# Kernel tuning notes

Measured on AMD Instinct MI355X. Metric: run time of the kernel, lower is better.

The kernel has to match this reference:

```python
import jax, jax.numpy as jnp
import numpy as np

B, S, H = 16, 8192, 256


def setup_inputs() -> dict:
    key = jax.random.key(0)
    k1, k2, k3, k4, k5, k6 = jax.random.split(key, 6)
    # He/Glorot-ish scaling for the linear layer is irrelevant for correctness; use small randn.
    return {
        "query": jax.random.normal(k1, (B, 1, H), dtype=jnp.float32),
        "key": jax.random.normal(k2, (B, S, H), dtype=jnp.float32),
        "value": jax.random.normal(k3, (B, S, H), dtype=jnp.float32),
        "W_attn": jax.random.normal(k4, (H, 2 * H), dtype=jnp.float32) * 0.05,  # nn.Linear(2H, H).weight
        "b_attn": jax.random.normal(k5, (H,), dtype=jnp.float32) * 0.05,
        "v": jax.random.uniform(k6, (H,), dtype=jnp.float32),  # torch.rand init
    }


def reference(query, key, value, W_attn, b_attn, v):
    # Faithful to: tanh(Linear(cat([query.repeat(S), key], -1))) @ v -> softmax -> weighted sum.
    # Split the Linear weight so we never materialize the repeated/concatenated [B,S,2H] tensor:
    # cat([q,k]) @ W.T == q @ Wq.T + k @ Wk.T, with Wq = W[:, :H], Wk = W[:, H:].
    Wq = W_attn[:, :H]  # [H, H]
    Wk = W_attn[:, H:]  # [H, H]
    hidden = jnp.tanh(
        jnp.einsum("bqh,oh->bqo", query, Wq)        # [B,1,H], broadcasts over S
        + jnp.einsum("bsh,oh->bso", key, Wk)        # [B,S,H]
        + b_attn
    )  # [B,S,H]
    scores = jnp.einsum("bsh,h->bs", hidden, v)      # [B,S]
    attn_weights = jax.nn.softmax(scores, axis=-1)   # softmax over sequence
    context = jnp.einsum("bs,bsh->bh", attn_weights, value)[:, None, :]  # [B,1,H]
    return context, attn_weights
```

## Files before the change

### kernel.cpp

```cpp
#include <hip/hip_runtime.h>

#define B_SZ 16
#define S_SZ 8192
#define H_SZ 256

typedef _Float16 half8 __attribute__((ext_vector_type(8)));
typedef float f32x4 __attribute__((ext_vector_type(4)));

__device__ __forceinline__ float tanh_fast(float x) {
  float e = __expf(2.0f * x);
  return 1.0f - 2.0f / (e + 1.0f);
}

__global__ __launch_bounds__(256) void prep_kernel(
    const float* __restrict__ query, const float* __restrict__ W_attn,
    const float* __restrict__ b_attn, float* __restrict__ qb) {
  const int b = blockIdx.x;
  const int jo = blockIdx.y;
  const int wid = threadIdx.x >> 6;
  const int lane = threadIdx.x & 63;
  const float4 q4 = *(const float4*)(query + b * H_SZ + lane * 4);
#pragma unroll 4
  for (int i = 0; i < 16; i++) {
    const int o = jo * 64 + wid * 16 + i;
    const float4 w = *(const float4*)(W_attn + (size_t)o * 512 + lane * 4);
    float p = q4.x * w.x + q4.y * w.y + q4.z * w.z + q4.w * w.w;
#pragma unroll
    for (int off = 32; off >= 1; off >>= 1) p += __shfl_xor(p, off, 64);
    if (lane == 0) qb[b * H_SZ + o] = p + b_attn[o];
  }
}

__global__ __launch_bounds__(512, 4) void scores_kernel(
    const float* __restrict__ key, const float* __restrict__ W_attn,
    const float* __restrict__ qb, const float* __restrict__ vvec,
    float* __restrict__ scores) {
  __shared__ _Float16 lds[64 * 264];

  const int tid = threadIdx.x;
  const int wid = tid >> 6;
  const int lane = tid & 63;
  const int n = lane & 15;
  const int quad = lane >> 4;
  const int rowBase = blockIdx.x * 128;
  const int b = rowBase >> 13;
  const int r = rowBase + wid * 16 + n;

  const float* krow = key + (size_t)r * H_SZ + quad * 8;
  half8 afrag[8];
#pragma unroll
  for (int ks = 0; ks < 8; ks++) {
    const float4* p = (const float4*)(krow + ks * 32);
    float4 f0 = p[0];
    float4 f1 = p[1];
    half8 a;
    a[0] = (_Float16)f0.x; a[1] = (_Float16)f0.y;
    a[2] = (_Float16)f0.z; a[3] = (_Float16)f0.w;
    a[4] = (_Float16)f1.x; a[5] = (_Float16)f1.y;
    a[6] = (_Float16)f1.z; a[7] = (_Float16)f1.w;
    afrag[ks] = a;
  }

  float score[4] = {0.f, 0.f, 0.f, 0.f};

  for (int c = 0; c < 4; c++) {
    __syncthreads();
    for (int idx = tid; idx < 2048; idx += 512) {
      int row = idx >> 5, seg = idx & 31;
      const float4* src =
          (const float4*)(W_attn + (size_t)(c * 64 + row) * 512 + 256 + seg * 8);
      float4 f0 = src[0];
      float4 f1 = src[1];
      half8 h;
      h[0] = (_Float16)f0.x; h[1] = (_Float16)f0.y;
      h[2] = (_Float16)f0.z; h[3] = (_Float16)f0.w;
      h[4] = (_Float16)f1.x; h[5] = (_Float16)f1.y;
      h[6] = (_Float16)f1.z; h[7] = (_Float16)f1.w;
      *(half8*)&lds[row * 264 + seg * 8] = h;
    }
    __syncthreads();

    f32x4 acc[4];
#pragma unroll
    for (int t = 0; t < 4; t++) {
      f32x4 z = {0.f, 0.f, 0.f, 0.f};
      acc[t] = z;
    }

#pragma unroll
    for (int ks = 0; ks < 8; ks++) {
#pragma unroll
      for (int t = 0; t < 4; t++) {
        half8 bfrag =
            *(const half8*)&lds[(t * 16 + n) * 264 + ks * 32 + quad * 8];
        acc[t] = __builtin_amdgcn_mfma_f32_16x16x32_f16(afrag[ks], bfrag,
                                                        acc[t], 0, 0, 0);
      }
    }

#pragma unroll
    for (int t = 0; t < 4; t++) {
      const int tt = c * 4 + t;
      const float qbv = qb[b * H_SZ + tt * 16 + n];
      const float vv = vvec[tt * 16 + n];
#pragma unroll
      for (int rg = 0; rg < 4; rg++) {
        float hv = tanh_fast(qbv + acc[t][rg]);
        score[rg] = fmaf(vv, hv, score[rg]);
      }
    }
  }

#pragma unroll
  for (int rg = 0; rg < 4; rg++) {
#pragma unroll
    for (int m = 8; m >= 1; m >>= 1)
      score[rg] += __shfl_xor(score[rg], m, 64);
  }
  if (n == 0) {
#pragma unroll
    for (int rg = 0; rg < 4; rg++)
      scores[rowBase + wid * 16 + quad * 4 + rg] = score[rg];
  }
}

__global__ __launch_bounds__(1024) void softmax_kernel(float* __restrict__ attn) {
  const int b = blockIdx.x;
  const int tid = threadIdx.x;
  float* w = attn + b * S_SZ;

  float vals[8];
  float m = -1e30f;
#pragma unroll
  for (int i = 0; i < 8; i++) {
    vals[i] = w[tid + (i << 10)];
    m = fmaxf(m, vals[i]);
  }
#pragma unroll
  for (int off = 32; off >= 1; off >>= 1) m = fmaxf(m, __shfl_xor(m, off, 64));

  __shared__ float red[16];
  __shared__ float bcast[2];
  const int wid = tid >> 6;
  const int lane = tid & 63;
  if (lane == 0) red[wid] = m;
  __syncthreads();
  if (wid == 0) {
    float mm = red[lane & 15];
#pragma unroll
    for (int off = 8; off >= 1; off >>= 1) mm = fmaxf(mm, __shfl_xor(mm, off, 64));
    if (lane == 0) bcast[0] = mm;
  }
  __syncthreads();
  m = bcast[0];

  float sum = 0.f;
#pragma unroll
  for (int i = 0; i < 8; i++) {
    vals[i] = __expf(vals[i] - m);
    sum += vals[i];
  }
#pragma unroll
  for (int off = 32; off >= 1; off >>= 1) sum += __shfl_xor(sum, off, 64);
  if (lane == 0) red[wid] = sum;
  __syncthreads();
  if (wid == 0) {
    float ss = red[lane & 15];
#pragma unroll
    for (int off = 8; off >= 1; off >>= 1) ss += __shfl_xor(ss, off, 64);
    if (lane == 0) bcast[1] = ss;
  }
  __syncthreads();
  const float inv = 1.0f / bcast[1];
#pragma unroll
  for (int i = 0; i < 8; i++) w[tid + (i << 10)] = vals[i] * inv;
}

__global__ __launch_bounds__(256) void context_kernel(
    const float* __restrict__ attn, const float* __restrict__ value,
    float* __restrict__ ctx) {
  const int b = blockIdx.x;
  const int j = blockIdx.y;
  const int h = threadIdx.x;
  const int s0 = j * 128;
  const float* w = attn + b * S_SZ + s0;
  const float* vp = value + ((size_t)(b * S_SZ + s0)) * H_SZ + h;
  float acc = 0.f;
#pragma unroll 8
  for (int s = 0; s < 128; s++) acc = fmaf(w[s], vp[(size_t)s * H_SZ], acc);
  atomicAdd(&ctx[b * H_SZ + h], acc);
}

extern "C" void kernel_launch(void* const* d_in, const int* in_sizes, int n_in,
                              void* d_out, int out_size, void* d_ws,
                              size_t ws_size, hipStream_t stream) {
  const float* query = (const float*)d_in[0];
  const float* key = (const float*)d_in[1];
  const float* value = (const float*)d_in[2];
  const float* W_attn = (const float*)d_in[3];
  const float* b_attn = (const float*)d_in[4];
  const float* vvec = (const float*)d_in[5];

  float* out = (float*)d_out;
  float* ctx = out;
  float* attn = out + 4096;

  prep_kernel<<<dim3(B_SZ, 4), 256, 0, stream>>>(query, W_attn, b_attn, ctx);
  scores_kernel<<<1024, 512, 0, stream>>>(key, W_attn, ctx, vvec, attn);
  hipMemsetAsync(ctx, 0, 4096 * sizeof(float), stream);
  softmax_kernel<<<B_SZ, 1024, 0, stream>>>(attn);
  context_kernel<<<dim3(B_SZ, 64), 256, 0, stream>>>(attn, value, ctx);
}
```

Measured before the change: 339.3 us.

## Enlarge score tiles, swizzle LDS, fuse softmax normalization into context kernel

```diff
diff --git a/kernel.cpp b/kernel.cpp
--- a/kernel.cpp
+++ b/kernel.cpp
@@ -31,44 +31,48 @@
   }
 }
 
-__global__ __launch_bounds__(512, 4) void scores_kernel(
+__global__ __launch_bounds__(1024, 4) void scores_kernel(
     const float* __restrict__ key, const float* __restrict__ W_attn,
     const float* __restrict__ qb, const float* __restrict__ vvec,
     float* __restrict__ scores) {
-  __shared__ _Float16 lds[64 * 264];
+  __shared__ _Float16 lds[128 * 256];
 
   const int tid = threadIdx.x;
   const int wid = tid >> 6;
   const int lane = tid & 63;
   const int n = lane & 15;
   const int quad = lane >> 4;
-  const int rowBase = blockIdx.x * 128;
-  const int b = rowBase >> 13;
-  const int r = rowBase + wid * 16 + n;
-
-  const float* krow = key + (size_t)r * H_SZ + quad * 8;
-  half8 afrag[8];
-#pragma unroll
-  for (int ks = 0; ks < 8; ks++) {
-    const float4* p = (const float4*)(krow + ks * 32);
-    float4 f0 = p[0];
-    float4 f1 = p[1];
-    half8 a;
-    a[0] = (_Float16)f0.x; a[1] = (_Float16)f0.y;
-    a[2] = (_Float16)f0.z; a[3] = (_Float16)f0.w;
-    a[4] = (_Float16)f1.x; a[5] = (_Float16)f1.y;
-    a[6] = (_Float16)f1.z; a[7] = (_Float16)f1.w;
-    afrag[ks] = a;
-  }
-
-  float score[4] = {0.f, 0.f, 0.f, 0.f};
-
-  for (int c = 0; c < 4; c++) {
-    __syncthreads();
-    for (int idx = tid; idx < 2048; idx += 512) {
+  const int wbase = (blockIdx.x * 16 + wid) * 32;
+  const int b = wbase >> 13;
+
+  half8 afrag[2][8];
+#pragma unroll
+  for (int rt = 0; rt < 2; rt++) {
+    const float* krow = key + (size_t)(wbase + rt * 16 + n) * H_SZ + quad * 8;
+#pragma unroll
+    for (int ks = 0; ks < 8; ks++) {
+      const float4* p = (const float4*)(krow + ks * 32);
+      float4 f0 = p[0];
+      float4 f1 = p[1];
+      half8 a;
+      a[0] = (_Float16)f0.x; a[1] = (_Float16)f0.y;
+      a[2] = (_Float16)f0.z; a[3] = (_Float16)f0.w;
+      a[4] = (_Float16)f1.x; a[5] = (_Float16)f1.y;
+      a[6] = (_Float16)f1.z; a[7] = (_Float16)f1.w;
+      afrag[rt][ks] = a;
+    }
+  }
+
+  float score[2][4] = {{0.f, 0.f, 0.f, 0.f}, {0.f, 0.f, 0.f, 0.f}};
+
+  for (int c = 0; c < 2; c++) {
+    if (c) __syncthreads();
+#pragma unroll
+    for (int it = 0; it < 4; it++) {
+      int idx = tid + it * 1024;
       int row = idx >> 5, seg = idx & 31;
       const float4* src =
-          (const float4*)(W_attn + (size_t)(c * 64 + row) * 512 + 256 + seg * 8);
+          (const float4*)(W_attn + (size_t)(c * 128 + row) * 512 + 256 + seg * 8);
       float4 f0 = src[0];
       float4 f1 = src[1];
       half8 h;
@@ -76,64 +80,63 @@
       h[2] = (_Float16)f0.z; h[3] = (_Float16)f0.w;
       h[4] = (_Float16)f1.x; h[5] = (_Float16)f1.y;
       h[6] = (_Float16)f1.z; h[7] = (_Float16)f1.w;
-      *(half8*)&lds[row * 264 + seg * 8] = h;
+      *(half8*)&lds[row * 256 + ((seg ^ (row & 31)) << 3)] = h;
     }
     __syncthreads();
 
-    f32x4 acc[4];
-#pragma unroll
-    for (int t = 0; t < 4; t++) {
-      f32x4 z = {0.f, 0.f, 0.f, 0.f};
-      acc[t] = z;
-    }
-
-#pragma unroll
-    for (int ks = 0; ks < 8; ks++) {
-#pragma unroll
-      for (int t = 0; t < 4; t++) {
-        half8 bfrag =
-            *(const half8*)&lds[(t * 16 + n) * 264 + ks * 32 + quad * 8];
-        acc[t] = __builtin_amdgcn_mfma_f32_16x16x32_f16(afrag[ks], bfrag,
-                                                        acc[t], 0, 0, 0);
+    for (int trow = 0; trow < 8; trow++) {
+      const int t = c * 8 + trow;
+      const int lrow = trow * 16 + n;
+      const int rl5 = lrow & 31;
+      f32x4 acc0 = {0.f, 0.f, 0.f, 0.f};
+      f32x4 acc1 = {0.f, 0.f, 0.f, 0.f};
+#pragma unroll
+      for (int ks = 0; ks < 8; ks++) {
+        const int seg = ks * 4 + quad;
+        half8 bfrag = *(const half8*)&lds[lrow * 256 + ((seg ^ rl5) << 3)];
+        acc0 = __builtin_amdgcn_mfma_f32_16x16x32_f16(afrag[0][ks], bfrag,
+                                                      acc0, 0, 0, 0);
+        acc1 = __builtin_amdgcn_mfma_f32_16x16x32_f16(afrag[1][ks], bfrag,
+                                                      acc1, 0, 0, 0);
       }
-    }
-
-#pragma unroll
-    for (int t = 0; t < 4; t++) {
-      const int tt = c * 4 + t;
-      const float qbv = qb[b * H_SZ + tt * 16 + n];
-      const float vv = vvec[tt * 16 + n];
+      const float qbv = qb[b * H_SZ + t * 16 + n];
+      const float vv = vvec[t * 16 + n];
 #pragma unroll
       for (int rg = 0; rg < 4; rg++) {
-        float hv = tanh_fast(qbv + acc[t][rg]);
-        score[rg] = fmaf(vv, hv, score[rg]);
+        score[0][rg] = fmaf(vv, tanh_fast(qbv + acc0[rg]), score[0][rg]);
+        score[1][rg] = fmaf(vv, tanh_fast(qbv + acc1[rg]), score[1][rg]);
       }
     }
   }
 
 #pragma unroll
-  for (int rg = 0; rg < 4; rg++) {
-#pragma unroll
-    for (int m = 8; m >= 1; m >>= 1)
-      score[rg] += __shfl_xor(score[rg], m, 64);
-  }
+  for (int rt = 0; rt < 2; rt++)
+#pragma unroll
+    for (int rg = 0; rg < 4; rg++)
+#pragma unroll
+      for (int m = 8; m >= 1; m >>= 1)
+        score[rt][rg] += __shfl_xor(score[rt][rg], m, 64);
   if (n == 0) {
 #pragma unroll
-    for (int rg = 0; rg < 4; rg++)
-      scores[rowBase + wid * 16 + quad * 4 + rg] = score[rg];
-  }
-}
-
-__global__ __launch_bounds__(1024) void softmax_kernel(float* __restrict__ attn) {
+    for (int rt = 0; rt < 2; rt++)
+#pragma unroll
+      for (int rg = 0; rg < 4; rg++)
+        scores[wbase + rt * 16 + quad * 4 + rg] = score[rt][rg];
+  }
+}
+
+__global__ __launch_bounds__(1024) void reduce_kernel(
+    const float* __restrict__ scores, float* __restrict__ mz,
+    float* __restrict__ ctx) {
   const int b = blockIdx.x;
   const int tid = threadIdx.x;
-  float* w = attn + b * S_SZ;
+  const float* s = scores + b * S_SZ;
 
   float vals[8];
   float m = -1e30f;
 #pragma unroll
   for (int i = 0; i < 8; i++) {
-    vals[i] = w[tid + (i << 10)];
+    vals[i] = s[tid + (i << 10)];
     m = fmaxf(m, vals[i]);
   }
 #pragma unroll
@@ -148,7 +151,8 @@
   if (wid == 0) {
     float mm = red[lane & 15];
 #pragma unroll
-    for (int off = 8; off >= 1; off >>= 1) mm = fmaxf(mm, __shfl_xor(mm, off, 64));
+    for (int off = 8; off >= 1; off >>= 1)
+      mm = fmaxf(mm, __shfl_xor(mm, off, 64));
     if (lane == 0) bcast[0] = mm;
   }
   __syncthreads();
@@ -156,10 +160,7 @@
 
   float sum = 0.f;
 #pragma unroll
-  for (int i = 0; i < 8; i++) {
-    vals[i] = __expf(vals[i] - m);
-    sum += vals[i];
-  }
+  for (int i = 0; i < 8; i++) sum += __expf(vals[i] - m);
 #pragma unroll
   for (int off = 32; off >= 1; off >>= 1) sum += __shfl_xor(sum, off, 64);
   if (lane == 0) red[wid] = sum;
@@ -168,26 +169,34 @@
     float ss = red[lane & 15];
 #pragma unroll
     for (int off = 8; off >= 1; off >>= 1) ss += __shfl_xor(ss, off, 64);
-    if (lane == 0) bcast[1] = ss;
-  }
-  __syncthreads();
-  const float inv = 1.0f / bcast[1];
-#pragma unroll
-  for (int i = 0; i < 8; i++) w[tid + (i << 10)] = vals[i] * inv;
+    if (lane == 0) {
+      bcast[1] = ss;
+      mz[2 * b] = m;
+      mz[2 * b + 1] = 1.0f / ss;
+    }
+  }
+  if (tid < H_SZ) ctx[b * H_SZ + tid] = 0.f;
 }
 
 __global__ __launch_bounds__(256) void context_kernel(
-    const float* __restrict__ attn, const float* __restrict__ value,
-    float* __restrict__ ctx) {
+    const float* __restrict__ mz, const float* __restrict__ value,
+    float* __restrict__ attn, float* __restrict__ ctx) {
+  __shared__ float wsm[256];
   const int b = blockIdx.x;
   const int j = blockIdx.y;
   const int h = threadIdx.x;
-  const int s0 = j * 128;
-  const float* w = attn + b * S_SZ + s0;
+  const int s0 = j * 256;
+  const float m = mz[2 * b];
+  const float invZ = mz[2 * b + 1];
+  float* arow = attn + b * S_SZ + s0;
+  const float w = __expf(arow[h] - m) * invZ;
+  arow[h] = w;
+  wsm[h] = w;
+  __syncthreads();
   const float* vp = value + ((size_t)(b * S_SZ + s0)) * H_SZ + h;
   float acc = 0.f;
 #pragma unroll 8
-  for (int s = 0; s < 128; s++) acc = fmaf(w[s], vp[(size_t)s * H_SZ], acc);
+  for (int s = 0; s < 256; s++) acc = fmaf(wsm[s], vp[(size_t)s * H_SZ], acc);
   atomicAdd(&ctx[b * H_SZ + h], acc);
 }
 
@@ -204,10 +213,10 @@
   float* out = (float*)d_out;
   float* ctx = out;
   float* attn = out + 4096;
+  float* mz = (float*)d_ws;
 
   prep_kernel<<<dim3(B_SZ, 4), 256, 0, stream>>>(query, W_attn, b_attn, ctx);
-  scores_kernel<<<1024, 512, 0, stream>>>(key, W_attn, ctx, vvec, attn);
-  hipMemsetAsync(ctx, 0, 4096 * sizeof(float), stream);
-  softmax_kernel<<<B_SZ, 1024, 0, stream>>>(attn);
-  context_kernel<<<dim3(B_SZ, 64), 256, 0, stream>>>(attn, value, ctx);
-}
+  scores_kernel<<<256, 1024, 0, stream>>>(key, W_attn, ctx, vvec, attn);
+  reduce_kernel<<<B_SZ, 1024, 0, stream>>>(attn, mz, ctx);
+  context_kernel<<<dim3(B_SZ, 32), 256, 0, stream>>>(mz, value, attn, ctx);
+}
```

Result: no change. 336.6 us (-0.8%).

## Swap MFMA operands, double-buffer key tiles, and fuse softmax max into scores

Applied to the files above, without the earlier changes.

```diff
diff --git a/kernel.cpp b/kernel.cpp
--- a/kernel.cpp
+++ b/kernel.cpp
@@ -12,9 +12,19 @@
   return 1.0f - 2.0f / (e + 1.0f);
 }
 
+__device__ __forceinline__ unsigned map_f(float f) {
+  unsigned u = __float_as_uint(f);
+  return (u & 0x80000000u) ? ~u : (u | 0x80000000u);
+}
+__device__ __forceinline__ float unmap_f(unsigned u) {
+  unsigned b = (u & 0x80000000u) ? (u ^ 0x80000000u) : ~u;
+  return __uint_as_float(b);
+}
+
 __global__ __launch_bounds__(256) void prep_kernel(
     const float* __restrict__ query, const float* __restrict__ W_attn,
-    const float* __restrict__ b_attn, float* __restrict__ qb) {
+    const float* __restrict__ b_attn, float* __restrict__ qb,
+    unsigned* __restrict__ mzu, float* __restrict__ Zf) {
   const int b = blockIdx.x;
   const int jo = blockIdx.y;
   const int wid = threadIdx.x >> 6;
@@ -29,166 +39,184 @@
     for (int off = 32; off >= 1; off >>= 1) p += __shfl_xor(p, off, 64);
     if (lane == 0) qb[b * H_SZ + o] = p + b_attn[o];
   }
-}
-
-__global__ __launch_bounds__(512, 4) void scores_kernel(
+  if (jo == 0 && threadIdx.x == 0) {
+    mzu[b] = 0u;
+    Zf[b] = 0.f;
+  }
+}
+
+__global__ __launch_bounds__(1024, 4) void scores_kernel(
     const float* __restrict__ key, const float* __restrict__ W_attn,
     const float* __restrict__ qb, const float* __restrict__ vvec,
-    float* __restrict__ scores) {
-  __shared__ _Float16 lds[64 * 264];
+    float* __restrict__ scores, unsigned* __restrict__ mzu) {
+  __shared__ _Float16 kbuf[2][32 * 256];
+  __shared__ float psum[2][32];
 
   const int tid = threadIdx.x;
   const int wid = tid >> 6;
   const int lane = tid & 63;
   const int n = lane & 15;
   const int quad = lane >> 4;
-  const int rowBase = blockIdx.x * 128;
+  const int rowBase = blockIdx.x * 256;
   const int b = rowBase >> 13;
-  const int r = rowBase + wid * 16 + n;
-
-  const float* krow = key + (size_t)r * H_SZ + quad * 8;
+
   half8 afrag[8];
-#pragma unroll
-  for (int ks = 0; ks < 8; ks++) {
-    const float4* p = (const float4*)(krow + ks * 32);
-    float4 f0 = p[0];
-    float4 f1 = p[1];
-    half8 a;
-    a[0] = (_Float16)f0.x; a[1] = (_Float16)f0.y;
-    a[2] = (_Float16)f0.z; a[3] = (_Float16)f0.w;
-    a[4] = (_Float16)f1.x; a[5] = (_Float16)f1.y;
-    a[6] = (_Float16)f1.z; a[7] = (_Float16)f1.w;
-    afrag[ks] = a;
-  }
-
-  float score[4] = {0.f, 0.f, 0.f, 0.f};
-
-  for (int c = 0; c < 4; c++) {
+  {
+    const float* wrow = W_attn + (size_t)(wid * 16 + n) * 512 + 256 + quad * 8;
+#pragma unroll
+    for (int ks = 0; ks < 8; ks++) {
+      float4 f0 = *(const float4*)(wrow + ks * 32);
+      float4 f1 = *(const float4*)(wrow + ks * 32 + 4);
+      half8 a;
+      a[0] = (_Float16)f0.x; a[1] = (_Float16)f0.y;
+      a[2] = (_Float16)f0.z; a[3] = (_Float16)f0.w;
+      a[4] = (_Float16)f1.x; a[5] = (_Float16)f1.y;
+      a[6] = (_Float16)f1.z; a[7] = (_Float16)f1.w;
+      afrag[ks] = a;
+    }
+  }
+  float qbv[4], vvv[4];
+#pragma unroll
+  for (int rg = 0; rg < 4; rg++) {
+    qbv[rg] = qb[b * H_SZ + wid * 16 + quad * 4 + rg];
+    vvv[rg] = vvec[wid * 16 + quad * 4 + rg];
+  }
+
+  if (tid < 64) ((float*)psum)[tid] = 0.f;
+
+  const int srow = tid >> 5;
+  const int sseg = tid & 31;
+  const size_t sbase = (size_t)(rowBase + srow) * H_SZ + sseg * 8;
+  const int sdst = srow * 256 + ((sseg ^ srow) << 3);
+
+  {
+    float4 f0 = *(const float4*)(key + sbase);
+    float4 f1 = *(const float4*)(key + sbase + 4);
+    half8 h;
+    h[0] = (_Float16)f0.x; h[1] = (_Float16)f0.y;
+    h[2] = (_Float16)f0.z; h[3] = (_Float16)f0.w;
+    h[4] = (_Float16)f1.x; h[5] = (_Float16)f1.y;
+    h[6] = (_Float16)f1.z; h[7] = (_Float16)f1.w;
+    *(half8*)&kbuf[0][sdst] = h;
+  }
+  __syncthreads();
+
+  float pmax = -1e30f;
+
+  for (int c = 0; c < 8; c++) {
+    float4 g0, g1;
+    if (c < 7) {
+      const size_t nb = sbase + (size_t)(c + 1) * 32 * H_SZ;
+      g0 = *(const float4*)(key + nb);
+      g1 = *(const float4*)(key + nb + 4);
+    }
+    const _Float16* kb = kbuf[c & 1];
+#pragma unroll
+    for (int rt = 0; rt < 2; rt++) {
+      const int lrow = rt * 16 + n;
+      f32x4 acc = {0.f, 0.f, 0.f, 0.f};
+#pragma unroll
+      for (int ks = 0; ks < 8; ks++) {
+        half8 bfrag =
+            *(const half8*)&kb[lrow * 256 + (((ks * 4 + quad) ^ lrow) << 3)];
+        acc = __builtin_amdgcn_mfma_f32_16x16x32_f16(afrag[ks], bfrag, acc,
+                                                     0, 0, 0);
+      }
+      float p = 0.f;
+#pragma unroll
+      for (int rg = 0; rg < 4; rg++)
+        p = fmaf(vvv[rg], tanh_fast(qbv[rg] + acc[rg]), p);
+      p += __shfl_xor(p, 16, 64);
+      p += __shfl_xor(p, 32, 64);
+      if (quad == 0) atomicAdd(&psum[c & 1][lrow], p);
+    }
+    if (c < 7) {
+      half8 h;
+      h[0] = (_Float16)g0.x; h[1] = (_Float16)g0.y;
+      h[2] = (_Float16)g0.z; h[3] = (_Float16)g0.w;
+      h[4] = (_Float16)g1.x; h[5] = (_Float16)g1.y;
+      h[6] = (_Float16)g1.z; h[7] = (_Float16)g1.w;
+      *(half8*)&kbuf[(c + 1) & 1][sdst] = h;
+    }
     __syncthreads();
-    for (int idx = tid; idx < 2048; idx += 512) {
-      int row = idx >> 5, seg = idx & 31;
-      const float4* src =
-          (const float4*)(W_attn + (size_t)(c * 64 + row) * 512 + 256 + seg * 8);
-      float4 f0 = src[0];
-      float4 f1 = src[1];
-      half8 h;
-      h[0] = (_Float16)f0.x; h[1] = (_Float16)f0.y;
-      h[2] = (_Float16)f0.z; h[3] = (_Float16)f0.w;
-      h[4] = (_Float16)f1.x; h[5] = (_Float16)f1.y;
-      h[6] = (_Float16)f1.z; h[7] = (_Float16)f1.w;
-      *(half8*)&lds[row * 264 + seg * 8] = h;
-    }
-    __syncthreads();
-
-    f32x4 acc[4];
-#pragma unroll
-    for (int t = 0; t < 4; t++) {
-      f32x4 z = {0.f, 0.f, 0.f, 0.f};
-      acc[t] = z;
-    }
-
-#pragma unroll
-    for (int ks = 0; ks < 8; ks++) {
-#pragma unroll
-      for (int t = 0; t < 4; t++) {
-        half8 bfrag =
-            *(const half8*)&lds[(t * 16 + n) * 264 + ks * 32 + quad * 8];
-        acc[t] = __builtin_amdgcn_mfma_f32_16x16x32_f16(afrag[ks], bfrag,
-                                                        acc[t], 0, 0, 0);
-      }
-    }
-
-#pragma unroll
-    for (int t = 0; t < 4; t++) {
-      const int tt = c * 4 + t;
-      const float qbv = qb[b * H_SZ + tt * 16 + n];
-      const float vv = vvec[tt * 16 + n];
-#pragma unroll
-      for (int rg = 0; rg < 4; rg++) {
-        float hv = tanh_fast(qbv + acc[t][rg]);
-        score[rg] = fmaf(vv, hv, score[rg]);
-      }
-    }
-  }
-
-#pragma unroll
-  for (int rg = 0; rg < 4; rg++) {
-#pragma unroll
-    for (int m = 8; m >= 1; m >>= 1)
-      score[rg] += __shfl_xor(score[rg], m, 64);
-  }
-  if (n == 0) {
-#pragma unroll
-    for (int rg = 0; rg < 4; rg++)
-      scores[rowBase + wid * 16 + quad * 4 + rg] = score[rg];
-  }
-}
-
-__global__ __launch_bounds__(1024) void softmax_kernel(float* __restrict__ attn) {
-  const int b = blockIdx.x;
+    if (tid < 32) {
+      float val = psum[c & 1][tid];
+      scores[rowBase + c * 32 + tid] = val;
+      pmax = fmaxf(pmax, val);
+      psum[c & 1][tid] = 0.f;
+    }
+  }
+  if (wid == 0) {
+#pragma unroll
+    for (int off = 32; off >= 1; off >>= 1)
+      pmax = fmaxf(pmax, __shfl_xor(pmax, off, 64));
+    if (lane == 0) atomicMax(&mzu[b], map_f(pmax));
+  }
+}
+
+__global__ __launch_bounds__(256) void reduce_kernel(
+    const float* __restrict__ scores, const unsigned* __restrict__ mzu,
+    float* __restrict__ Zf, float* __restrict__ ctx) {
+  const int b = blockIdx.x >> 4;
+  const int j = blockIdx.x & 15;
   const int tid = threadIdx.x;
-  float* w = attn + b * S_SZ;
-
-  float vals[8];
-  float m = -1e30f;
-#pragma unroll
-  for (int i = 0; i < 8; i++) {
-    vals[i] = w[tid + (i << 10)];
-    m = fmaxf(m, vals[i]);
-  }
-#pragma unroll
-  for (int off = 32; off >= 1; off >>= 1) m = fmaxf(m, __shfl_xor(m, off, 64));
-
-  __shared__ float red[16];
-  __shared__ float bcast[2];
-  const int wid = tid >> 6;
-  const int lane = tid & 63;
-  if (lane == 0) red[wid] = m;
-  __syncthreads();
-  if (wid == 0) {
-    float mm = red[lane & 15];
-#pragma unroll
-    for (int off = 8; off >= 1; off >>= 1) mm = fmaxf(mm, __shfl_xor(mm, off, 64));
-    if (lane == 0) bcast[0] = mm;
-  }
-  __syncthreads();
-  m = bcast[0];
-
-  float sum = 0.f;
-#pragma unroll
-  for (int i = 0; i < 8; i++) {
-    vals[i] = __expf(vals[i] - m);
-    sum += vals[i];
-  }
-#pragma unroll
-  for (int off = 32; off >= 1; off >>= 1) sum += __shfl_xor(sum, off, 64);
-  if (lane == 0) red[wid] = sum;
-  __syncthreads();
-  if (wid == 0) {
-    float ss = red[lane & 15];
-#pragma unroll
-    for (int off = 8; off >= 1; off >>= 1) ss += __shfl_xor(ss, off, 64);
-    if (lane == 0) bcast[1] = ss;
-  }
-  __syncthreads();
-  const float inv = 1.0f / bcast[1];
-#pragma unroll
-  for (int i = 0; i < 8; i++) w[tid + (i << 10)] = vals[i] * inv;
+  const float m = unmap_f(mzu[b]);
+  const float* s = scores + b * S_SZ + j * 512;
+  float part = __expf(s[tid] - m) + __expf(s[tid + 256] - m);
+#pragma unroll
+  for (int off = 32; off >= 1; off >>= 1) part += __shfl_xor(part, off, 64);
+  __shared__ float red[4];
+  if ((tid & 63) == 0) red[tid >> 6] = part;
+  __syncthreads();
+  if (tid == 0) atomicAdd(&Zf[b], red[0] + red[1] + red[2] + red[3]);
+  if (tid < 16) ctx[b * H_SZ + j * 16 + tid] = 0.f;
 }
 
 __global__ __launch_bounds__(256) void context_kernel(
-    const float* __restrict__ attn, const float* __restrict__ value,
+    const unsigned* __restrict__ mzu, const float* __restrict__ Zf,
+    const float* __restrict__ value, float* __restrict__ attn,
     float* __restrict__ ctx) {
+  __shared__ float wsm[256];
+  __shared__ float4 psum4[3][64];
   const int b = blockIdx.x;
   const int j = blockIdx.y;
-  const int h = threadIdx.x;
-  const int s0 = j * 128;
-  const float* w = attn + b * S_SZ + s0;
-  const float* vp = value + ((size_t)(b * S_SZ + s0)) * H_SZ + h;
-  float acc = 0.f;
+  const int t = threadIdx.x;
+  const int g = t >> 6;
+  const int hl = t & 63;
+  const int s0 = j * 256;
+  const float m = unmap_f(mzu[b]);
+  const float invZ = 1.0f / Zf[b];
+  float* arow = attn + b * S_SZ + s0;
+  const float w = __expf(arow[t] - m) * invZ;
+  arow[t] = w;
+  wsm[t] = w;
+  __syncthreads();
+  const float4* vp =
+      (const float4*)value + ((size_t)(b * S_SZ + s0 + g * 64)) * 64 + hl;
+  float4 acc = {0.f, 0.f, 0.f, 0.f};
 #pragma unroll 8
-  for (int s = 0; s < 128; s++) acc = fmaf(w[s], vp[(size_t)s * H_SZ], acc);
-  atomicAdd(&ctx[b * H_SZ + h], acc);
+  for (int s = 0; s < 64; s++) {
+    const float ww = wsm[g * 64 + s];
+    const float4 vv = vp[(size_t)s * 64];
+    acc.x = fmaf(ww, vv.x, acc.x);
+    acc.y = fmaf(ww, vv.y, acc.y);
+    acc.z = fmaf(ww, vv.z, acc.z);
+    acc.w = fmaf(ww, vv.w, acc.w);
+  }
+  if (g > 0) psum4[g - 1][hl] = acc;
+  __syncthreads();
+  if (g == 0) {
+    const float4 a1 = psum4[0][hl], a2 = psum4[1][hl], a3 = psum4[2][hl];
+    acc.x += a1.x + a2.x + a3.x;
+    acc.y += a1.y + a2.y + a3.y;
+    acc.z += a1.z + a2.z + a3.z;
+    acc.w += a1.w + a2.w + a3.w;
+    float* cp = ctx + b * H_SZ + hl * 4;
+    atomicAdd(cp + 0, acc.x);
+    atomicAdd(cp + 1, acc.y);
+    atomicAdd(cp + 2, acc.z);
+    atomicAdd(cp + 3, acc.w);
+  }
 }
 
 extern "C" void kernel_launch(void* const* d_in, const int* in_sizes, int n_in,
@@ -204,10 +232,13 @@
   float* out = (float*)d_out;
   float* ctx = out;
   float* attn = out + 4096;
-
-  prep_kernel<<<dim3(B_SZ, 4), 256, 0, stream>>>(query, W_attn, b_attn, ctx);
-  scores_kernel<<<1024, 512, 0, stream>>>(key, W_attn, ctx, vvec, attn);
-  hipMemsetAsync(ctx, 0, 4096 * sizeof(float), stream);
-  softmax_kernel<<<B_SZ, 1024, 0, stream>>>(attn);
-  context_kernel<<<dim3(B_SZ, 64), 256, 0, stream>>>(attn, value, ctx);
-}
+  unsigned* mzu = (unsigned*)d_ws;
+  float* Zf = (float*)d_ws + 16;
+
+  prep_kernel<<<dim3(B_SZ, 4), 256, 0, stream>>>(query, W_attn, b_attn, ctx,
+                                                 mzu, Zf);
+  scores_kernel<<<512, 1024, 0, stream>>>(key, W_attn, ctx, vvec, attn, mzu);
+  reduce_kernel<<<256, 256, 0, stream>>>(attn, mzu, Zf, ctx);
+  context_kernel<<<dim3(B_SZ, 32), 256, 0, stream>>>(mzu, Zf, value, attn,
+                                                     ctx);
+}
```

Measured after the change: 324.3 us. 4.4% less time.
